# Kernel tuning notes

Hardware: AMD Instinct MI355X
Metric: run time of the kernel (lower is better)

The kernel has to match this reference:

```python
import jax, jax.numpy as jnp
import numpy as np

B, S, H = 2, 2048, 3072
NH, NKV, HD = 16, 16, 256
Q_SIZE = NH * HD          # 4096
KV_SIZE = NKV * HD        # 4096
ROPE_THETA = 10000.0


def setup_inputs() -> dict:
    key = jax.random.key(0)
    k1, k2, k3 = jax.random.split(key, 3)
    hidden_states = jax.random.normal(k1, (B, S, H), dtype=jnp.float32)
    positions = jnp.arange(B * S, dtype=jnp.int32).reshape(B, S) % S  # 0..S-1 per row
    Wqkv = jax.random.normal(k2, (H, Q_SIZE + 2 * KV_SIZE), dtype=jnp.float32) * 0.02
    Wo = jax.random.normal(k3, (Q_SIZE, H), dtype=jnp.float32) * 0.02
    return {"hidden_states": hidden_states, "positions": positions, "Wqkv": Wqkv, "Wo": Wo}


def _apply_rope_neox(x, positions, head_dim, theta):
    # x: [B, S, nheads, head_dim]; neox style: rotate halves
    half = head_dim // 2
    inv_freq = 1.0 / (theta ** (jnp.arange(0, head_dim, 2, dtype=jnp.float32) / head_dim))  # [half]
    angles = positions.astype(jnp.float32)[..., None] * inv_freq  # [B, S, half]
    cos = jnp.cos(angles)[:, :, None, :]  # [B, S, 1, half]
    sin = jnp.sin(angles)[:, :, None, :]
    x1, x2 = x[..., :half], x[..., half:]
    return jnp.concatenate([x1 * cos - x2 * sin, x2 * cos + x1 * sin], axis=-1)


def reference(hidden_states, positions, Wqkv, Wo):
    # fused QKV projection (bias-free)
    qkv = jnp.einsum('bsh,hd->bsd', hidden_states, Wqkv)
    q, k, v = jnp.split(qkv, [Q_SIZE, Q_SIZE + KV_SIZE], axis=-1)
    q = q.reshape(B, S, NH, HD)
    k = k.reshape(B, S, NKV, HD)
    v = v.reshape(B, S, NKV, HD)
    # RoPE (neox style, rotary_dim == head_dim)
    q = _apply_rope_neox(q, positions, HD, ROPE_THETA)
    k = _apply_rope_neox(k, positions, HD, ROPE_THETA)
    # GQA: repeat kv heads if fewer than query heads
    if NKV != NH:
        rep = NH // NKV
        k = jnp.repeat(k, rep, axis=2)
        v = jnp.repeat(v, rep, axis=2)
    scale = float(HD) ** -0.5
    scores = jnp.einsum('bqhd,bkhd->bhqk', q, k) * scale  # [B, NH, S, S]
    causal = jnp.tril(jnp.ones((S, S), dtype=bool))
    scores = jnp.where(causal[None, None], scores, jnp.finfo(scores.dtype).min)
    probs = jax.nn.softmax(scores, axis=-1)
    attn = jnp.einsum('bhqk,bkhd->bqhd', probs, v).reshape(B, S, Q_SIZE)
    return jnp.einsum('bsd,dh->bsh', attn, Wo)
```

## Files before the change

### kernel.cpp

```cpp
#include <hip/hip_runtime.h>

#define SQLEN 2048
#define QKVW 12288
#define NHEADS 16
#define HEADD 256

typedef unsigned short u16;
typedef __bf16 bf16x8 __attribute__((ext_vector_type(8)));
typedef float f32x4 __attribute__((ext_vector_type(4)));

__device__ __forceinline__ float bf2f(u16 u) {
  union { unsigned int i; float f; } v; v.i = ((unsigned int)u) << 16; return v.f;
}
__device__ __forceinline__ u16 f2bf(float f) {
  union { float f; unsigned int i; } v; v.f = f;
  unsigned int x = v.i;
  return (u16)((x + 0x7fffu + ((x >> 16) & 1u)) >> 16);
}

__device__ __forceinline__ void gl_lds16(const u16* g, u16* l) {
  __builtin_amdgcn_global_load_lds(
      (const __attribute__((address_space(1))) void*)g,
      (__attribute__((address_space(3))) void*)l, 16, 0, 0);
}

__global__ __launch_bounds__(256) void f32_to_bf16(
    const float* __restrict__ src, u16* __restrict__ dst) {
  long i = (long)(blockIdx.x * 256 + threadIdx.x) * 8;
  float4 a = *reinterpret_cast<const float4*>(src + i);
  float4 b = *reinterpret_cast<const float4*>(src + i + 4);
  u16 tmp[8] = {f2bf(a.x), f2bf(a.y), f2bf(a.z), f2bf(a.w),
                f2bf(b.x), f2bf(b.y), f2bf(b.z), f2bf(b.w)};
  *reinterpret_cast<uint4*>(dst + i) = *reinterpret_cast<uint4*>(tmp);
}

__global__ __launch_bounds__(256) void ktranspose_f32(
    const float* __restrict__ src, u16* __restrict__ dst,
    int src_ld, int dst_ld) {
  __shared__ __align__(16) u16 t[64][64];
  const int c0 = blockIdx.x * 64, r0 = blockIdx.y * 64;
  const int tid = threadIdx.x;
  #pragma unroll
  for (int it = 0; it < 2; ++it) {
    int c = tid + it * 256;
    int r = c >> 3, ch = c & 7;
    const float* sp = src + (long)(r0 + r) * src_ld + c0 + ch * 8;
    float4 v0 = *reinterpret_cast<const float4*>(sp);
    float4 v1 = *reinterpret_cast<const float4*>(sp + 4);
    u16 tmp[8] = {f2bf(v0.x), f2bf(v0.y), f2bf(v0.z), f2bf(v0.w),
                  f2bf(v1.x), f2bf(v1.y), f2bf(v1.z), f2bf(v1.w)};
    int sw = ch ^ (r & 7);
    *reinterpret_cast<uint4*>(&t[r][sw * 8]) = *reinterpret_cast<uint4*>(tmp);
  }
  __syncthreads();
  #pragma unroll
  for (int it = 0; it < 2; ++it) {
    int c = tid + it * 256;
    int rr = c >> 3, ch = c & 7;
    u16 tmp[8];
    #pragma unroll
    for (int j = 0; j < 8; ++j) {
      int k = ch * 8 + j;
      int sw = (rr >> 3) ^ (k & 7);
      tmp[j] = t[k][sw * 8 + (rr & 7)];
    }
    *reinterpret_cast<uint4*>(dst + (long)(c0 + rr) * dst_ld + r0 + ch * 8) =
        *reinterpret_cast<uint4*>(tmp);
  }
}

__global__ __launch_bounds__(256) void ktranspose_bf16(
    const u16* __restrict__ src, u16* __restrict__ dst,
    int src_ld, int dst_ld, long src_off,
    long szs1, long szs2, long dzs1, long dzs2) {
  __shared__ __align__(16) u16 t[64][64];
  const int z = blockIdx.z;
  const u16* s = src + src_off + (long)(z >> 4) * szs1 + (long)(z & 15) * szs2;
  u16* d = dst + (long)(z >> 4) * dzs1 + (long)(z & 15) * dzs2;
  const int c0 = blockIdx.x * 64, r0 = blockIdx.y * 64;
  const int tid = threadIdx.x;
  #pragma unroll
  for (int it = 0; it < 2; ++it) {
    int c = tid + it * 256;
    int r = c >> 3, ch = c & 7;
    uint4 v = *reinterpret_cast<const uint4*>(s + (long)(r0 + r) * src_ld + c0 + ch * 8);
    int sw = ch ^ (r & 7);
    *reinterpret_cast<uint4*>(&t[r][sw * 8]) = v;
  }
  __syncthreads();
  #pragma unroll
  for (int it = 0; it < 2; ++it) {
    int c = tid + it * 256;
    int rr = c >> 3, ch = c & 7;
    u16 tmp[8];
    #pragma unroll
    for (int j = 0; j < 8; ++j) {
      int k = ch * 8 + j;
      int sw = (rr >> 3) ^ (k & 7);
      tmp[j] = t[k][sw * 8 + (rr & 7)];
    }
    *reinterpret_cast<uint4*>(d + (long)(c0 + rr) * dst_ld + r0 + ch * 8) =
        *reinterpret_cast<uint4*>(tmp);
  }
}

template <typename OUT_T>
__global__ __launch_bounds__(512, 2) void gemm_bt8(
    const u16* __restrict__ A, const u16* __restrict__ BT, OUT_T* __restrict__ C,
    int M, int N, int K) {
  (void)M;
  __shared__ __align__(16) u16 As[2][256][64];
  __shared__ __align__(16) u16 Bs[2][256][64];
  const int tid = threadIdx.x;
  const int wave = tid >> 6, lane = tid & 63;
  const int quad = lane >> 4, l16 = lane & 15;
  const int wm = (wave >> 2) * 128, wn = (wave & 3) * 64;
  const int gx = gridDim.x;
  const int flat = blockIdx.y * gx + blockIdx.x;
  const int cpx = (gx * gridDim.y) >> 3;
  const int virt = (flat & 7) * cpx + (flat >> 3);
  const long m0 = (long)(virt / gx) * 256, n0 = (long)(virt % gx) * 256;
  const int sw = l16 & 7;
  const int ca0 = (quad ^ sw) * 8;
  const int ca1 = ((4 + quad) ^ sw) * 8;
  const int srow = tid >> 3;
  const int sdst8 = (tid & 7) * 8;
  const int ssrc8 = ((tid & 7) ^ (srow & 7)) * 8;
  const long Kl = K;
  const u16* gA = A + (m0 + srow) * Kl + ssrc8;
  const u16* gB = BT + (n0 + srow) * Kl + ssrc8;
  const int nt = K >> 6;

  f32x4 acc[8][4] = {};
  bf16x8 af[4][2];
  bf16x8 bfr[4][2];

#define STAGE_A(BB, R, K0) \
  gl_lds16(gA + (long)((R) << 6) * Kl + (K0), &As[BB][((R) << 6) + srow][sdst8])
#define STAGE_B(BB, R, K0) \
  gl_lds16(gB + (long)((R) << 6) * Kl + (K0), &Bs[BB][((R) << 6) + srow][sdst8])
#define READ_A(BB, RBASE)                                              \
  _Pragma("unroll") for (int i4 = 0; i4 < 4; ++i4) {                   \
    const u16* p_ = &As[BB][(RBASE) + i4 * 16 + l16][0];               \
    af[i4][0] = *reinterpret_cast<const bf16x8*>(p_ + ca0);            \
    af[i4][1] = *reinterpret_cast<const bf16x8*>(p_ + ca1);            \
  }
#define READ_B(BB, JB)                                                 \
  _Pragma("unroll") for (int j2 = 0; j2 < 2; ++j2) {                   \
    const u16* p_ = &Bs[BB][wn + ((JB) + j2) * 16 + l16][0];           \
    bfr[(JB) + j2][0] = *reinterpret_cast<const bf16x8*>(p_ + ca0);    \
    bfr[(JB) + j2][1] = *reinterpret_cast<const bf16x8*>(p_ + ca1);    \
  }
#define QUADMFMA(MB, NB)                                               \
  _Pragma("unroll") for (int i4 = 0; i4 < 4; ++i4)                     \
  _Pragma("unroll") for (int j2 = 0; j2 < 2; ++j2)                     \
  _Pragma("unroll") for (int s = 0; s < 2; ++s)                        \
    acc[(MB) + i4][(NB) + j2] = __builtin_amdgcn_mfma_f32_16x16x32_bf16( \
        af[i4][s], bfr[(NB) + j2][s], acc[(MB) + i4][(NB) + j2], 0, 0, 0);
#define BAR() asm volatile("s_barrier" ::: "memory")
#define LGKM0() asm volatile("s_waitcnt lgkmcnt(0)" ::: "memory")

  STAGE_A(0, 0, 0); STAGE_A(0, 1, 0); STAGE_A(0, 2, 0); STAGE_A(0, 3, 0);
  STAGE_B(0, 0, 0); STAGE_B(0, 1, 0); STAGE_B(0, 2, 0); STAGE_B(0, 3, 0);
  if (nt > 1) {
    STAGE_A(1, 0, 64); STAGE_A(1, 2, 64);
    STAGE_B(1, 0, 64); STAGE_B(1, 1, 64);
    STAGE_A(1, 1, 64); STAGE_A(1, 3, 64);
    asm volatile("s_waitcnt vmcnt(6)" ::: "memory");
  } else {
    asm volatile("s_waitcnt vmcnt(0)" ::: "memory");
  }
  BAR();

  for (int t = 0; t < nt; ++t) {
    const int b = t & 1;
    const long kn = (long)(t + 1) << 6;
    const long kn2 = (long)(t + 2) << 6;
    const bool st1 = (t + 1 < nt), st2 = (t + 2 < nt);
    READ_A(b, wm);
    READ_B(b, 0);
    if (st1) { STAGE_B(b ^ 1, 2, kn); STAGE_B(b ^ 1, 3, kn); }
    asm volatile("s_waitcnt lgkmcnt(8)" ::: "memory");
    BAR(); LGKM0();
    __builtin_amdgcn_s_setprio(1);
    QUADMFMA(0, 0);
    __builtin_amdgcn_s_setprio(0);
    BAR();
    READ_B(b, 2);
    if (st2) { STAGE_A(b, 0, kn2); STAGE_A(b, 2, kn2); }
    BAR(); LGKM0();
    __builtin_amdgcn_s_setprio(1);
    QUADMFMA(0, 2);
    __builtin_amdgcn_s_setprio(0);
    BAR();
    READ_A(b, wm + 64);
    if (st2) { STAGE_B(b, 0, kn2); STAGE_B(b, 1, kn2); }
    BAR(); LGKM0();
    __builtin_amdgcn_s_setprio(1);
    QUADMFMA(4, 2);
    __builtin_amdgcn_s_setprio(0);
    BAR();
    if (st2) { STAGE_A(b, 1, kn2); STAGE_A(b, 3, kn2); }
    BAR();
    __builtin_amdgcn_s_setprio(1);
    QUADMFMA(4, 0);
    __builtin_amdgcn_s_setprio(0);
    if (st2)      asm volatile("s_waitcnt vmcnt(6)" ::: "memory");
    else if (st1) asm volatile("s_waitcnt vmcnt(0)" ::: "memory");
    BAR();
  }

  #pragma unroll
  for (int i = 0; i < 8; ++i)
    #pragma unroll
    for (int j = 0; j < 4; ++j) {
      long col = n0 + wn + j * 16 + l16;
      #pragma unroll
      for (int r = 0; r < 4; ++r) {
        long row = m0 + wm + i * 16 + quad * 4 + r;
        if constexpr (sizeof(OUT_T) == 4)
          C[row * (long)N + col] = acc[i][j][r];
        else
          C[row * (long)N + col] = f2bf(acc[i][j][r]);
      }
    }
#undef STAGE_A
#undef STAGE_B
#undef READ_A
#undef READ_B
#undef QUADMFMA
#undef BAR
#undef LGKM0
}

__global__ __launch_bounds__(256) void rope_kernel(
    u16* __restrict__ qkv, const int* __restrict__ positions) {
  int idx = blockIdx.x * 256 + threadIdx.x;
  int i = idx & 127;
  int head = (idx >> 7) & 31;
  int row = idx >> 12;
  int col = (head < NHEADS) ? head * HEADD : 4096 + (head - NHEADS) * HEADD;
  u16* p = qkv + (long)row * QKVW + col;
  float x1 = bf2f(p[i]), x2 = bf2f(p[i + 128]);
  float pos = (float)positions[row];
  float inv_freq = exp2f((float)i * (-13.287712379549449f / 128.0f));
  float ang = pos * inv_freq;
  float sv, cv;
  sincosf(ang, &sv, &cv);
  p[i] = f2bf(x1 * cv - x2 * sv);
  p[i + 128] = f2bf(x2 * cv + x1 * sv);
}

__global__ __launch_bounds__(256, 1) void attn_kernel(
    const u16* __restrict__ qkv, const u16* __restrict__ VT,
    u16* __restrict__ attnout) {
  const int s_hw = blockIdx.y * 16 + blockIdx.x;
  const int xcd = s_hw & 7, idx = s_hw >> 3;
  const int bh = xcd * 4 + (idx >> 4);
  const int p = idx & 15;
  const int b = bh >> 4, h = bh & 15;
  const int tid = threadIdx.x;
  const int wave = tid >> 6, lane = tid & 63;
  const int quad = lane >> 4, l16 = lane & 15;
  const int sw7 = l16 & 7;

  __shared__ __align__(16) u16 Ks[2][64][256];
  __shared__ __align__(16) u16 Vs[2][256][64];
  __shared__ __align__(16) u16 Ps[64][72];

  const u16* qp = qkv + (long)b * SQLEN * QKVW + h * HEADD;
  const u16* kp = qp + 4096;
  const u16* vtp = VT + (long)bh * HEADD * SQLEN;
  const float cs = 0.0625f * 1.4426950408889634f;

  const u16* ksrc = kp + (long)(tid >> 5) * QKVW + ((tid & 31) ^ ((tid >> 5) & 7)) * 8;
  const u16* vsrc = vtp + (long)(tid >> 3) * SQLEN + ((tid & 7) ^ ((tid >> 3) & 7)) * 8;
  u16* kdst = &Ks[0][0][0] + tid * 8;
  u16* vdst = &Vs[0][0][0] + tid * 8;

#define STAGE_K(KT, BB) { const u16* gk_ = ksrc + (long)(KT) * 64 * QKVW;      \
  _Pragma("unroll") for (int it = 0; it < 8; ++it)                             \
    gl_lds16(gk_ + (long)it * 8 * QKVW, kdst + (BB) * 16384 + it * 2048); }
#define STAGE_V(KT, BB) { const u16* gv_ = vsrc + (KT) * 64;                   \
  _Pragma("unroll") for (int it = 0; it < 8; ++it)                             \
    gl_lds16(gv_ + (long)it * 32 * SQLEN, vdst + (BB) * 16384 + it * 2048); }
#define ABAR() asm volatile("s_barrier" ::: "memory")

  for (int half = 0; half < 2; ++half) {
    const int qt = half ? p : 31 - p;

    ABAR();
    const u16* qrow = qp + (long)(qt * 64 + wave * 16 + l16) * QKVW + quad * 8;
    bf16x8 qf[8];
    #pragma unroll
    for (int s = 0; s < 8; ++s)
      qf[s] = *reinterpret_cast<const bf16x8*>(qrow + s * 32);

    STAGE_K(0, 0); STAGE_V(0, 0);
    if (qt > 0) {
      STAGE_K(1, 1); STAGE_V(1, 1);
      asm volatile("s_waitcnt vmcnt(16)" ::: "memory");
    } else {
      asm volatile("s_waitcnt vmcnt(0)" ::: "memory");
    }
    ABAR();

    float m_i[4], l_i[4];
    #pragma unroll
    for (int r = 0; r < 4; ++r) { m_i[r] = -INFINITY; l_i[r] = 0.f; }
    f32x4 o[16] = {};

    for (int kt = 0; kt <= qt; ++kt) {
      const int bb = kt & 1;
      f32x4 sc[4] = {};
      __builtin_amdgcn_s_setprio(1);
      #pragma unroll
      for (int s = 0; s < 8; ++s) {
        #pragma unroll
        for (int nb = 0; nb < 4; ++nb) {
          bf16x8 kf = *reinterpret_cast<const bf16x8*>(
              &Ks[bb][nb * 16 + l16][(((s << 2) + quad) ^ sw7) * 8]);
          sc[nb] = __builtin_amdgcn_mfma_f32_16x16x32_bf16(qf[s], kf, sc[nb], 0, 0, 0);
        }
      }
      __builtin_amdgcn_s_setprio(0);
      const bool diag = (kt == qt);
      #pragma unroll
      for (int nb = 0; nb < 4; ++nb)
        #pragma unroll
        for (int r = 0; r < 4; ++r) {
          float v = sc[nb][r] * cs;
          if (diag) {
            int colL = nb * 16 + l16, rowL = wave * 16 + quad * 4 + r;
            if (colL > rowL) v = -INFINITY;
          }
          sc[nb][r] = v;
        }
      float alpha[4];
      #pragma unroll
      for (int r = 0; r < 4; ++r) {
        float t = fmaxf(fmaxf(sc[0][r], sc[1][r]), fmaxf(sc[2][r], sc[3][r]));
        #pragma unroll
        for (int d = 1; d < 16; d <<= 1) t = fmaxf(t, __shfl_xor(t, d));
        float mn = fmaxf(m_i[r], t);
        alpha[r] = exp2f(m_i[r] - mn);
        m_i[r] = mn;
      }
      #pragma unroll
      for (int r = 0; r < 4; ++r) {
        float t = 0.f;
        #pragma unroll
        for (int nb = 0; nb < 4; ++nb) {
          float pr = exp2f(sc[nb][r] - m_i[r]);
          sc[nb][r] = pr;
          t += pr;
        }
        #pragma unroll
        for (int d = 1; d < 16; d <<= 1) t += __shfl_xor(t, d);
        l_i[r] = l_i[r] * alpha[r] + t;
      }
      ABAR();
      if (kt + 2 <= qt) STAGE_K(kt + 2, bb);
      #pragma unroll
      for (int nb = 0; nb < 4; ++nb)
        #pragma unroll
        for (int r = 0; r < 4; ++r)
          Ps[wave * 16 + quad * 4 + r][nb * 16 + l16] = f2bf(sc[nb][r]);
      #pragma unroll
      for (int c16 = 0; c16 < 16; ++c16)
        #pragma unroll
        for (int r = 0; r < 4; ++r)
          o[c16][r] *= alpha[r];
      bf16x8 pf[2];
      #pragma unroll
      for (int s2 = 0; s2 < 2; ++s2)
        pf[s2] = *reinterpret_cast<const bf16x8*>(&Ps[wave * 16 + l16][s2 * 32 + quad * 8]);
      __builtin_amdgcn_s_setprio(1);
      #pragma unroll
      for (int c16 = 0; c16 < 16; ++c16) {
        #pragma unroll
        for (int s2 = 0; s2 < 2; ++s2) {
          bf16x8 vf = *reinterpret_cast<const bf16x8*>(
              &Vs[bb][c16 * 16 + l16][(((s2 << 2) + quad) ^ sw7) * 8]);
          o[c16] = __builtin_amdgcn_mfma_f32_16x16x32_bf16(pf[s2], vf, o[c16], 0, 0, 0);
        }
      }
      __builtin_amdgcn_s_setprio(0);
      if (kt < qt) {
        ABAR();
        if (kt + 2 <= qt) {
          STAGE_V(kt + 2, bb);
          asm volatile("s_waitcnt vmcnt(16)" ::: "memory");
        } else {
          asm volatile("s_waitcnt vmcnt(0)" ::: "memory");
        }
        ABAR();
      }
    }
    #pragma unroll
    for (int r = 0; r < 4; ++r) {
      float inv = 1.0f / l_i[r];
      long q = qt * 64 + wave * 16 + quad * 4 + r;
      long rowoff = ((long)b * SQLEN + q) * 4096 + h * HEADD;
      #pragma unroll
      for (int c16 = 0; c16 < 16; ++c16)
        attnout[rowoff + c16 * 16 + l16] = f2bf(o[c16][r] * inv);
    }
  }
#undef STAGE_K
#undef STAGE_V
#undef ABAR
}

extern "C" void kernel_launch(void* const* d_in, const int* in_sizes, int n_in,
                              void* d_out, int out_size, void* d_ws, size_t ws_size,
                              hipStream_t stream) {
  const float* hidden = (const float*)d_in[0];
  const int* positions = (const int*)d_in[1];
  const float* Wqkv = (const float*)d_in[2];
  const float* Wo = (const float*)d_in[3];
  float* out = (float*)d_out;
  char* ws = (char*)d_ws;

  u16* qkv     = (u16*)(ws);
  u16* WqkvT   = (u16*)(ws + 100663296L);
  u16* attn    = (u16*)(ws + 100663296L);
  u16* WoT     = (u16*)(ws + 134217728L);
  u16* hiddenB = (u16*)(ws + 176160768L);
  u16* VT      = (u16*)(ws + 176160768L);

  f32_to_bf16<<<dim3(6144, 1, 1), 256, 0, stream>>>(hidden, hiddenB);
  ktranspose_f32<<<dim3(192, 48, 1), 256, 0, stream>>>(Wqkv, WqkvT, 12288, 3072);
  gemm_bt8<u16><<<dim3(48, 16, 1), 512, 0, stream>>>(
      hiddenB, WqkvT, qkv, 4096, 12288, 3072);
  rope_kernel<<<dim3(65536, 1, 1), 256, 0, stream>>>(qkv, positions);
  ktranspose_bf16<<<dim3(4, 32, 32), 256, 0, stream>>>(
      qkv, VT, 12288, 2048, 8192,
      25165824L, 256L, 8388608L, 524288L);
  attn_kernel<<<dim3(16, 32, 1), 256, 0, stream>>>(qkv, VT, attn);
  ktranspose_f32<<<dim3(48, 64, 1), 256, 0, stream>>>(Wo, WoT, 3072, 4096);
  gemm_bt8<float><<<dim3(12, 16, 1), 512, 0, stream>>>(
      attn, WoT, out, 4096, 3072, 4096);
}
```

Measured before the change: 996.9 us.

## Add lazy softmax rescaling, RoPE cos/sin table, and drop block-index swizzles

The attention kernel now rescales the output accumulator and running sum only when some row's new max exceeds the old max by more than 8 (log2 units), checked wave-wide. This skips the 64-element alpha multiply and exp on most tiles at the cost of a bounded growth in unnormalized values. RoPE cos/sin values are precomputed into a table indexed by position, so the per-element sincos is replaced by a table load. The XCD-aware block remapping in the GEMM and attention kernels is removed in favour of direct block indices, which may reduce L2 locality.

```diff
diff --git a/kernel.cpp b/kernel.cpp
--- a/kernel.cpp
+++ b/kernel.cpp
@@ -115,11 +115,7 @@
   const int wave = tid >> 6, lane = tid & 63;
   const int quad = lane >> 4, l16 = lane & 15;
   const int wm = (wave >> 2) * 128, wn = (wave & 3) * 64;
-  const int gx = gridDim.x;
-  const int flat = blockIdx.y * gx + blockIdx.x;
-  const int cpx = (gx * gridDim.y) >> 3;
-  const int virt = (flat & 7) * cpx + (flat >> 3);
-  const long m0 = (long)(virt / gx) * 256, n0 = (long)(virt % gx) * 256;
+  const long m0 = (long)blockIdx.y * 256, n0 = (long)blockIdx.x * 256;
   const int sw = l16 & 7;
   const int ca0 = (quad ^ sw) * 8;
   const int ca1 = ((4 + quad) ^ sw) * 8;
@@ -233,8 +229,19 @@
 #undef LGKM0
 }
 
+__global__ __launch_bounds__(256) void rope_table(float2* __restrict__ tab) {
+  int idx = blockIdx.x * 256 + threadIdx.x;
+  int pos = idx >> 7, i = idx & 127;
+  float inv_freq = exp2f((float)i * (-13.287712379549449f / 128.0f));
+  float ang = (float)pos * inv_freq;
+  float sv, cv;
+  sincosf(ang, &sv, &cv);
+  tab[idx] = make_float2(cv, sv);
+}
+
 __global__ __launch_bounds__(256) void rope_kernel(
-    u16* __restrict__ qkv, const int* __restrict__ positions) {
+    u16* __restrict__ qkv, const int* __restrict__ positions,
+    const float2* __restrict__ tab) {
   int idx = blockIdx.x * 256 + threadIdx.x;
   int i = idx & 127;
   int head = (idx >> 7) & 31;
@@ -242,22 +249,16 @@
   int col = (head < NHEADS) ? head * HEADD : 4096 + (head - NHEADS) * HEADD;
   u16* p = qkv + (long)row * QKVW + col;
   float x1 = bf2f(p[i]), x2 = bf2f(p[i + 128]);
-  float pos = (float)positions[row];
-  float inv_freq = exp2f((float)i * (-13.287712379549449f / 128.0f));
-  float ang = pos * inv_freq;
-  float sv, cv;
-  sincosf(ang, &sv, &cv);
-  p[i] = f2bf(x1 * cv - x2 * sv);
-  p[i + 128] = f2bf(x2 * cv + x1 * sv);
+  float2 cssn = tab[positions[row] * 128 + i];
+  p[i] = f2bf(x1 * cssn.x - x2 * cssn.y);
+  p[i + 128] = f2bf(x2 * cssn.x + x1 * cssn.y);
 }
 
 __global__ __launch_bounds__(256, 1) void attn_kernel(
     const u16* __restrict__ qkv, const u16* __restrict__ VT,
     u16* __restrict__ attnout) {
-  const int s_hw = blockIdx.y * 16 + blockIdx.x;
-  const int xcd = s_hw & 7, idx = s_hw >> 3;
-  const int bh = xcd * 4 + (idx >> 4);
-  const int p = idx & 15;
+  const int p = blockIdx.x;
+  const int bh = blockIdx.y;
   const int b = bh >> 4, h = bh & 15;
   const int tid = threadIdx.x;
   const int wave = tid >> 6, lane = tid & 63;
@@ -336,15 +337,30 @@
           }
           sc[nb][r] = v;
         }
-      float alpha[4];
+      float t4[4];
+      bool need = false;
       #pragma unroll
       for (int r = 0; r < 4; ++r) {
         float t = fmaxf(fmaxf(sc[0][r], sc[1][r]), fmaxf(sc[2][r], sc[3][r]));
         #pragma unroll
         for (int d = 1; d < 16; d <<= 1) t = fmaxf(t, __shfl_xor(t, d));
-        float mn = fmaxf(m_i[r], t);
-        alpha[r] = exp2f(m_i[r] - mn);
-        m_i[r] = mn;
+        t4[r] = t;
+        need = need || (t > m_i[r] + 8.0f);
+      }
+      if (__any(need)) {
+        float alpha[4];
+        #pragma unroll
+        for (int r = 0; r < 4; ++r) {
+          float mn = fmaxf(m_i[r], t4[r]);
+          alpha[r] = exp2f(m_i[r] - mn);
+          m_i[r] = mn;
+          l_i[r] *= alpha[r];
+        }
+        #pragma unroll
+        for (int c16 = 0; c16 < 16; ++c16)
+          #pragma unroll
+          for (int r = 0; r < 4; ++r)
+            o[c16][r] *= alpha[r];
       }
       #pragma unroll
       for (int r = 0; r < 4; ++r) {
@@ -357,7 +373,7 @@
         }
         #pragma unroll
         for (int d = 1; d < 16; d <<= 1) t += __shfl_xor(t, d);
-        l_i[r] = l_i[r] * alpha[r] + t;
+        l_i[r] += t;
       }
       ABAR();
       if (kt + 2 <= qt) STAGE_K(kt + 2, bb);
@@ -366,11 +382,6 @@
         #pragma unroll
         for (int r = 0; r < 4; ++r)
           Ps[wave * 16 + quad * 4 + r][nb * 16 + l16] = f2bf(sc[nb][r]);
-      #pragma unroll
-      for (int c16 = 0; c16 < 16; ++c16)
-        #pragma unroll
-        for (int r = 0; r < 4; ++r)
-          o[c16][r] *= alpha[r];
       bf16x8 pf[2];
       #pragma unroll
       for (int s2 = 0; s2 < 2; ++s2)
@@ -428,12 +439,14 @@
   u16* WoT     = (u16*)(ws + 134217728L);
   u16* hiddenB = (u16*)(ws + 176160768L);
   u16* VT      = (u16*)(ws + 176160768L);
+  float2* rtab = (float2*)(ws + 201326592L);
 
   f32_to_bf16<<<dim3(6144, 1, 1), 256, 0, stream>>>(hidden, hiddenB);
+  rope_table<<<dim3(1024, 1, 1), 256, 0, stream>>>(rtab);
   ktranspose_f32<<<dim3(192, 48, 1), 256, 0, stream>>>(Wqkv, WqkvT, 12288, 3072);
   gemm_bt8<u16><<<dim3(48, 16, 1), 512, 0, stream>>>(
       hiddenB, WqkvT, qkv, 4096, 12288, 3072);
-  rope_kernel<<<dim3(65536, 1, 1), 256, 0, stream>>>(qkv, positions);
+  rope_kernel<<<dim3(65536, 1, 1), 256, 0, stream>>>(qkv, positions, rtab);
   ktranspose_bf16<<<dim3(4, 32, 32), 256, 0, stream>>>(
       qkv, VT, 12288, 2048, 8192,
       25165824L, 256L, 8388608L, 524288L);
```

Result: slower. 1.050 ms (+5.3%).
